# Kernel tuning notes

Hardware: AMD Instinct MI355X
Metric: run time of the kernel (lower is better)

The kernel has to match this reference:

```python
import jax, jax.numpy as jnp
import numpy as np
import math

GAMMA = 0.97      # discounting
LAM = 0.95        # gae lambda
EPSILON = 0.3     # ppo clip
EPS = 0.2         # gpo clip (eps)
ENT_COST = 0.01
RSCALE = 1.0
ALPHA = 1.0
NUM_STEPS = 1.0e6 # normalization step count buffer


def _mlp(x, Ws, bs):
    for i, (W, b) in enumerate(zip(Ws, bs)):
        x = x @ W.T + b
        if i < len(Ws) - 1:
            x = jax.nn.silu(x)
    return x


def _dist_create(logits):
    loc, s = jnp.split(logits, 2, axis=-1)
    return loc, jax.nn.softplus(s) + 0.001


def _log_det_jac(x):
    # tanh bijector log|det J| per element
    return 2.0 * (math.log(2.0) - x - jax.nn.softplus(-2.0 * x))


def _log_prob(loc, scale, dist):
    lu = -0.5 * jnp.square((dist - loc) / scale)
    ln = 0.5 * math.log(2.0 * math.pi) + jnp.log(scale)
    return (lu - ln - _log_det_jac(dist)).sum(-1)


def _entropy(loc, scale, noise):
    ln = 0.5 * math.log(2.0 * math.pi) + jnp.log(scale)
    ent = (0.5 + ln) * jnp.ones_like(loc)
    dist = loc + scale * noise  # reparameterized sample (torch.normal)
    return (ent + _log_det_jac(dist)).sum(-1)


def _kl(pl, ps, ql, qs):
    vr = jnp.square(ps / qs)
    t1 = jnp.square((pl - ql) / qs)
    return (0.5 * (vr + t1 - 1.0 - jnp.log(vr))).mean(-1)


def _normalize(obs, rm, rv):
    var = jnp.clip(rv / (NUM_STEPS + 1.0), 1e-6, 1e6)
    return jnp.clip((obs - rm) / jnp.sqrt(var), -5.0, 5.0)


def _gae(truncation, termination, reward, values, bootstrap_value):
    tm = 1.0 - truncation
    v1 = jnp.concatenate([values[1:], bootstrap_value[None]], 0)
    deltas = (reward + GAMMA * (1.0 - termination) * v1 - values) * tm

    def step(acc, xs):
        d, te, tmask = xs
        acc = d + GAMMA * (1.0 - te) * tmask * LAM * acc
        return acc, acc

    _, vmx = jax.lax.scan(step, jnp.zeros_like(bootstrap_value),
                          (deltas, termination, tm), reverse=True)
    vs = vmx + values
    vs1 = jnp.concatenate([vs[1:], bootstrap_value[None]], 0)
    adv = (reward + GAMMA * (1.0 - termination) * vs1 - values) * tm
    return vs, adv


def _loss(observation, pobservation, reward, done, truncation, logits, action,
          noise, pw0, pb0, pw1, pb1, pw2, pb2, vw0, vb0, vw1, vb1, vw2, vb2,
          running_mean, running_variance, kl_coef):
    sg = jax.lax.stop_gradient
    Pw, Pb = [pw0, pw1, pw2], [pb0, pb1, pb2]
    Vw, Vb = [vw0, vw1, vw2], [vb0, vb1, vb2]

    obs_n = _normalize(observation, running_mean, running_variance)
    pobs_n = _normalize(pobservation, running_mean, running_variance)

    guider_logits = _mlp(obs_n[:-1], Pw, Pb)
    learner_logits = _mlp(pobs_n[:-1], Pw, Pb)
    baseline = _mlp(obs_n, Vw, Vb).squeeze(-1)  # [T+1, B]
    bootstrap = baseline[-1]
    baseline = baseline[:-1]

    reward_s = reward * RSCALE
    termination = done * (1.0 - truncation)

    loc, scale = _dist_create(logits)
    b_lp = _log_prob(loc, scale, action)
    gl, gs = _dist_create(guider_logits)
    g_lp = _log_prob(gl, gs, action)
    ll, ls = _dist_create(learner_logits)
    l_lp = _log_prob(ll, ls, action)

    kl_learner = _kl(sg(gl), sg(gs), ll, ls).mean()
    kl_guider = _kl(gl, gs, sg(ll), sg(ls))
    # use_clip = True branch
    diff = g_lp - l_lp
    m = jnp.where(diff > math.log(1.0 + EPS), 1.0,
                  jnp.where(diff < math.log(1.0 - EPS), 1.0, 0.0))
    kl_guider = (kl_guider * m).mean()

    vs, adv = _gae(truncation, termination, reward_s, sg(baseline), sg(bootstrap))
    vs = sg(vs)
    adv = sg((adv - adv.mean()) / (jnp.std(adv, ddof=1) + 1e-5))

    rho = jnp.exp(g_lp - b_lp)
    rho_clip = jnp.exp(jnp.clip(g_lp - sg(l_lp), math.log(1.0 - EPS), math.log(1.0 + EPS))
                       + sg(l_lp) - b_lp)
    rho_clip = jnp.clip(rho_clip, 1.0 - EPSILON, 1.0 + EPSILON)
    guider_policy_loss = -jnp.mean(jnp.minimum(rho * adv, rho_clip * adv))

    rho2 = jnp.exp(jnp.minimum(l_lp - b_lp, 10.0))  # stable_exp
    rho2c = jnp.clip(rho2, 1.0 - EPSILON, 1.0 + EPSILON)
    learner_policy_loss = -jnp.mean(jnp.minimum(rho2 * adv, rho2c * adv))

    v_err = vs - baseline
    v_loss = jnp.mean(v_err * v_err) * 0.25

    entropy = jnp.mean(_entropy(loc, scale, noise))
    entropy_loss = -ENT_COST * entropy

    learner_loss = kl_learner + learner_policy_loss * ALPHA  # use_clip
    guider_loss = kl_guider + guider_policy_loss
    total = learner_loss + guider_loss + v_loss + entropy_loss
    return total, guider_loss, learner_loss, kl_learner


def setup_inputs() -> dict:
    key = jax.random.key(0)
    T, B, OBS, ACT, H = 1024, 256, 64, 8, 256
    ks = iter(jax.random.split(key, 32))

    def lin(fin, fout):
        W = jax.random.normal(next(ks), (fout, fin), jnp.float32) / np.float32(np.sqrt(fin))
        b = jnp.zeros((fout,), jnp.float32)
        return W, b

    pw0, pb0 = lin(OBS, H); pw1, pb1 = lin(H, H); pw2, pb2 = lin(H, 2 * ACT)
    vw0, vb0 = lin(OBS, H); vw1, vb1 = lin(H, H); vw2, vb2 = lin(H, 1)

    observation = jax.random.normal(next(ks), (T + 1, B, OBS), jnp.float32)
    pobservation = observation + 0.1 * jax.random.normal(next(ks), (T + 1, B, OBS), jnp.float32)
    reward = jax.random.normal(next(ks), (T, B), jnp.float32)
    done = (jax.random.uniform(next(ks), (T, B)) < 0.01).astype(jnp.float32)
    truncation = (jax.random.uniform(next(ks), (T, B)) < 0.005).astype(jnp.float32)
    logits = 0.5 * jax.random.normal(next(ks), (T, B, 2 * ACT), jnp.float32)
    action = jax.random.normal(next(ks), (T, B, ACT), jnp.float32)
    noise = jax.random.normal(next(ks), (T, B, ACT), jnp.float32)
    running_mean = jnp.zeros((OBS,), jnp.float32)
    running_variance = jnp.ones((OBS,), jnp.float32) * NUM_STEPS  # unit variance after /num_steps
    kl_coef = jnp.ones((1,), jnp.float32)

    return {"observation": observation, "pobservation": pobservation,
            "reward": reward, "done": done, "truncation": truncation,
            "logits": logits, "action": action, "noise": noise,
            "pw0": pw0, "pb0": pb0, "pw1": pw1, "pb1": pb1, "pw2": pw2, "pb2": pb2,
            "vw0": vw0, "vb0": vb0, "vw1": vw1, "vb1": vb1, "vw2": vw2, "vb2": vb2,
            "running_mean": running_mean, "running_variance": running_variance,
            "kl_coef": kl_coef}


def reference(observation, pobservation, reward, done, truncation, logits, action,
              noise, pw0, pb0, pw1, pb1, pw2, pb2, vw0, vb0, vw1, vb1, vw2, vb2,
              running_mean, running_variance, kl_coef):
    return _loss(observation, pobservation, reward, done, truncation, logits,
                 action, noise, pw0, pb0, pw1, pb1, pw2, pb2, vw0, vb0, vw1, vb1,
                 vw2, vb2, running_mean, running_variance, kl_coef)
```

## Files before the change

kernel.cpp:

```cpp
#include <hip/hip_runtime.h>
#include <math.h>

#define GAMMA_   0.97f
#define LAM_     0.95f
#define EPSILON_ 0.3f
#define HLOG2PI_ 0.91893853320467274f
#define LOG2C_   0.69314718055994531f
#define LOG1P2_  0.18232155679395463f
#define LOG0P8_  (-0.22314355131420976f)

typedef unsigned short u16;
typedef unsigned int   u32;
typedef _Float16 half8 __attribute__((ext_vector_type(8)));
typedef _Float16 half4 __attribute__((ext_vector_type(4)));
typedef __attribute__((ext_vector_type(4))) float floatx4;
typedef __attribute__((ext_vector_type(8))) float floatx8;

constexpr int  TT     = 1024;
constexpr long ROWS_P = (long)TT * 256;
constexpr long ROWS_V = (long)(TT + 1) * 256;

constexpr long FR_W0P_HI = 0;
constexpr long FR_W0P_LO = 16384;
constexpr long FR_W1P_HI = 32768;
constexpr long FR_W1P_LO = 98304;
constexpr long FR_W2P_HI = 163840;
constexpr long FR_W2P_LO = 167936;
constexpr long FR_W0V_HI = 172032;
constexpr long FR_W0V_LO = 188416;
constexpr long FR_W1V_HI = 204800;
constexpr long FR_W1V_LO = 270336;
constexpr long FR_W2V_HI = 335872;
constexpr long FR_W2V_LO = 339968;
constexpr long FR_TOTAL  = 344064;

constexpr long WS_ACC  = 0;
constexpr long WS_INV  = 32;
constexpr long WS_ADV  = 96;
constexpr long WS_BASE = WS_ADV + ROWS_P;
constexpr long WS_GA   = WS_BASE + ROWS_V;
constexpr long WS_GP   = WS_GA + 8192;
constexpr long WS_GS   = WS_GP + 8192;
constexpr long WS_BANK = WS_GS + 8192;


__device__ __forceinline__ float softplus_f(float x) {
  return (x > 20.f) ? x : log1pf(expf(x));
}
__device__ __forceinline__ float silu_f(float x) {
  return x * __builtin_amdgcn_rcpf(1.f + __expf(-x));
}
__device__ __forceinline__ float clamp30(float x) {
  return fminf(1e30f, fmaxf(-1e30f, x));
}

__global__ void prep_kernel(const float* __restrict__ rv,
                            float* __restrict__ inv_std,
                            float* __restrict__ accum,
                            float* __restrict__ accumB) {
  int t = threadIdx.x;
  if (t < 32) accum[t] = 0.f;
  for (int i = t; i < 1024; i += 256) accumB[i] = 0.f;
  if (t < 64) {
    float var = rv[t] / 1000001.0f;
    var = fminf(1e6f, fmaxf(1e-6f, var));
    inv_std[t] = 1.f / sqrtf(var);
  }
}

__global__ void convert_kernel(const float* __restrict__ pw0,
                               const float* __restrict__ pw1,
                               const float* __restrict__ pw2,
                               const float* __restrict__ vw0,
                               const float* __restrict__ vw1,
                               const float* __restrict__ vw2,
                               u16* __restrict__ frag) {
  int idx = blockIdx.x * 256 + threadIdx.x;
  const float* W; int kslog, K, nvalid; long hioff, looff; int e;
  if (idx < 16384)       { W = pw0; e = idx;          kslog = 1; K = 64;  nvalid = 256; hioff = FR_W0P_HI; looff = FR_W0P_LO; }
  else if (idx < 81920)  { W = pw1; e = idx - 16384;  kslog = 3; K = 256; nvalid = 256; hioff = FR_W1P_HI; looff = FR_W1P_LO; }
  else if (idx < 86016)  { W = pw2; e = idx - 81920;  kslog = 3; K = 256; nvalid = 16;  hioff = FR_W2P_HI; looff = FR_W2P_LO; }
  else if (idx < 102400) { W = vw0; e = idx - 86016;  kslog = 1; K = 64;  nvalid = 256; hioff = FR_W0V_HI; looff = FR_W0V_LO; }
  else if (idx < 167936) { W = vw1; e = idx - 102400; kslog = 3; K = 256; nvalid = 256; hioff = FR_W1V_HI; looff = FR_W1V_LO; }
  else                   { W = vw2; e = idx - 167936; kslog = 3; K = 256; nvalid = 1;   hioff = FR_W2V_HI; looff = FR_W2V_LO; }
  int j    = e & 7;
  int lane = (e >> 3) & 63;
  int ks   = (e >> 9) & ((1 << kslog) - 1);
  int nt   = e >> (9 + kslog);
  int n = nt * 16 + (lane & 15);
  int k = ks * 32 + ((lane >> 4) << 3) + j;
  float w = (n < nvalid) ? W[n * K + k] : 0.f;
  _Float16 hi = (_Float16)w;
  _Float16 lo = (_Float16)(w - (float)hi);
  frag[hioff + e] = *(u16*)&hi;
  frag[looff + e] = *(u16*)&lo;
}

constexpr int SX = 72;
constexpr int SH = 264;

__global__ __launch_bounds__(256, 5)
void policy_kernel(const float* __restrict__ obs,
                   const float* __restrict__ pobs,
                   const float* __restrict__ rm,
                   const float* __restrict__ inv_std,
                   const u16* __restrict__ frag,
                   const float* __restrict__ b0,
                   const float* __restrict__ b1,
                   const float* __restrict__ b2,
                   const float* __restrict__ logits,
                   const float* __restrict__ action,
                   const float* __restrict__ noise,
                   const float* __restrict__ adv,
                   const float* __restrict__ accum,
                   float* __restrict__ accumB) {
  __shared__ __align__(16) _Float16 H[32 * SH];
  __shared__ __align__(16) float OUT2[2 * 32 * 16];
  __shared__ float red[80];

  const int tid  = threadIdx.x;
  const long row0 = (long)blockIdx.x * 16;
  const int lane = tid & 63;
  const int wv   = tid >> 6;
  const int lm   = lane & 15;
  const int lq   = lane >> 4;

  _Float16* X = H;

  {
    int vr = tid >> 3;
    int f0 = (tid & 7) * 8;
    const float* src = (vr < 16) ? obs : pobs;
    floatx8 v  = *(const floatx8*)&src[(row0 + (vr & 15)) * 64 + f0];
    floatx8 m  = *(const floatx8*)&rm[f0];
    floatx8 is = *(const floatx8*)&inv_std[f0];
    half8 h;
    #pragma unroll
    for (int j = 0; j < 8; ++j)
      h[j] = (_Float16)fminf(5.f, fmaxf(-5.f, (v[j] - m[j]) * is[j]));
    *(half8*)&X[vr * SX + f0] = h;
  }

  const int  er   = (tid >> 3) & 15;
  const int  ed   = tid & 7;
  const long erow = row0 + er;
  float pf_a   = action[erow * 8 + ed];
  float pf_loc = logits[erow * 16 + ed];
  float pf_sr  = logits[erow * 16 + 8 + ed];
  float pf_nd  = noise[erow * 8 + ed];
  float pf_adv = adv[erow];
  float pf_s3  = accum[3];
  float pf_s4  = accum[4];

  floatx4 acc[2][4];
  #pragma unroll
  for (int nt = 0; nt < 4; ++nt) {
    floatx4 bz = *(const floatx4*)&b0[(wv * 4 + nt) * 16 + lq * 4];
    acc[0][nt] = bz; acc[1][nt] = bz;
  }
  __syncthreads();

  {
    const half8* B0h = (const half8*)(frag + FR_W0P_HI);
    const half8* B0l = (const half8*)(frag + FR_W0P_LO);
    #pragma unroll
    for (int ks = 0; ks < 2; ++ks) {
      half8 Bh[4], Bl[4];
      #pragma unroll
      for (int nt = 0; nt < 4; ++nt) {
        int ntg = wv * 4 + nt;
        Bh[nt] = B0h[(ntg * 2 + ks) * 64 + lane];
        Bl[nt] = B0l[(ntg * 2 + ks) * 64 + lane];
      }
      half8 A0 = *(const half8*)&X[lm * SX + ks * 32 + lq * 8];
      half8 A1 = *(const half8*)&X[(16 + lm) * SX + ks * 32 + lq * 8];
      __builtin_amdgcn_s_setprio(1);
      #pragma unroll
      for (int nt = 0; nt < 4; ++nt) {
        acc[0][nt] = __builtin_amdgcn_mfma_f32_16x16x32_f16(Bh[nt], A0, acc[0][nt], 0, 0, 0);
        acc[1][nt] = __builtin_amdgcn_mfma_f32_16x16x32_f16(Bh[nt], A1, acc[1][nt], 0, 0, 0);
      }
      #pragma unroll
      for (int nt = 0; nt < 4; ++nt) {
        acc[0][nt] = __builtin_amdgcn_mfma_f32_16x16x32_f16(Bl[nt], A0, acc[0][nt], 0, 0, 0);
        acc[1][nt] = __builtin_amdgcn_mfma_f32_16x16x32_f16(Bl[nt], A1, acc[1][nt], 0, 0, 0);
      }
      __builtin_amdgcn_s_setprio(0);
    }
  }
  __syncthreads();

  #pragma unroll
  for (int nt = 0; nt < 4; ++nt) {
    int colbase = (wv * 4 + nt) * 16 + lq * 4;
    #pragma unroll
    for (int mt = 0; mt < 2; ++mt) {
      int row = mt * 16 + lm;
      half4 h;
      #pragma unroll
      for (int reg = 0; reg < 4; ++reg)
        h[reg] = (_Float16)silu_f(acc[mt][nt][reg]);
      *(half4*)&H[row * SH + colbase] = h;
    }
  }
  __syncthreads();

  {
    const half8* B1h = (const half8*)(frag + FR_W1P_HI);
    const half8* B1l = (const half8*)(frag + FR_W1P_LO);
    #pragma unroll
    for (int nt = 0; nt < 4; ++nt) {
      floatx4 bz = *(const floatx4*)&b1[(wv * 4 + nt) * 16 + lq * 4];
      acc[0][nt] = bz; acc[1][nt] = bz;
    }
    #pragma unroll 1
    for (int ks = 0; ks < 8; ++ks) {
      half8 Bh[4], Bl[4];
      #pragma unroll
      for (int nt = 0; nt < 4; ++nt) {
        int ntg = wv * 4 + nt;
        Bh[nt] = B1h[(ntg * 8 + ks) * 64 + lane];
        Bl[nt] = B1l[(ntg * 8 + ks) * 64 + lane];
      }
      half8 A0 = *(const half8*)&H[lm * SH + ks * 32 + lq * 8];
      half8 A1 = *(const half8*)&H[(16 + lm) * SH + ks * 32 + lq * 8];
      __builtin_amdgcn_s_setprio(1);
      #pragma unroll
      for (int nt = 0; nt < 4; ++nt) {
        acc[0][nt] = __builtin_amdgcn_mfma_f32_16x16x32_f16(Bh[nt], A0, acc[0][nt], 0, 0, 0);
        acc[1][nt] = __builtin_amdgcn_mfma_f32_16x16x32_f16(Bh[nt], A1, acc[1][nt], 0, 0, 0);
      }
      #pragma unroll
      for (int nt = 0; nt < 4; ++nt) {
        acc[0][nt] = __builtin_amdgcn_mfma_f32_16x16x32_f16(Bl[nt], A0, acc[0][nt], 0, 0, 0);
        acc[1][nt] = __builtin_amdgcn_mfma_f32_16x16x32_f16(Bl[nt], A1, acc[1][nt], 0, 0, 0);
      }
      __builtin_amdgcn_s_setprio(0);
    }
  }
  __syncthreads();

  #pragma unroll
  for (int nt = 0; nt < 4; ++nt) {
    int colbase = (wv * 4 + nt) * 16 + lq * 4;
    #pragma unroll
    for (int mt = 0; mt < 2; ++mt) {
      int row = mt * 16 + lm;
      half4 h;
      #pragma unroll
      for (int reg = 0; reg < 4; ++reg)
        h[reg] = (_Float16)silu_f(acc[mt][nt][reg]);
      *(half4*)&H[row * SH + colbase] = h;
    }
  }
  __syncthreads();

  {
    const half8* B2h = (const half8*)(frag + FR_W2P_HI);
    const half8* B2l = (const half8*)(frag + FR_W2P_LO);
    const int m3 = wv & 1, kh = wv >> 1;
    floatx4 c3a, c3b = (floatx4){0.f, 0.f, 0.f, 0.f};
    c3a = (kh == 0) ? *(const floatx4*)&b2[lq * 4] : (floatx4){0.f, 0.f, 0.f, 0.f};
    __builtin_amdgcn_s_setprio(1);
    #pragma unroll
    for (int j = 0; j < 4; j += 2) {
      int ks = kh * 4 + j;
      half8 A0 = *(const half8*)&H[(m3 * 16 + lm) * SH + ks * 32 + lq * 8];
      half8 A1 = *(const half8*)&H[(m3 * 16 + lm) * SH + (ks + 1) * 32 + lq * 8];
      c3a = __builtin_amdgcn_mfma_f32_16x16x32_f16(B2h[ks * 64 + lane],       A0, c3a, 0, 0, 0);
      c3b = __builtin_amdgcn_mfma_f32_16x16x32_f16(B2h[(ks + 1) * 64 + lane], A1, c3b, 0, 0, 0);
      c3a = __builtin_amdgcn_mfma_f32_16x16x32_f16(B2l[ks * 64 + lane],       A0, c3a, 0, 0, 0);
      c3b = __builtin_amdgcn_mfma_f32_16x16x32_f16(B2l[(ks + 1) * 64 + lane], A1, c3b, 0, 0, 0);
    }
    __builtin_amdgcn_s_setprio(0);
    *(floatx4*)&OUT2[kh * 512 + (m3 * 16 + lm) * 16 + lq * 4] = c3a + c3b;
  }
  __syncthreads();

  if (tid < 128) {
    int r = tid >> 3;
    int d = tid & 7;

    float gl  = OUT2[r * 16 + d]            + OUT2[512 + r * 16 + d];
    float gsr = OUT2[r * 16 + 8 + d]        + OUT2[512 + r * 16 + 8 + d];
    float ll  = OUT2[(16 + r) * 16 + d]     + OUT2[512 + (16 + r) * 16 + d];
    float lsr = OUT2[(16 + r) * 16 + 8 + d] + OUT2[512 + (16 + r) * 16 + 8 + d];
    float a   = pf_a;
    float loc = pf_loc;
    float sr  = pf_sr;
    float nd  = pf_nd;

    float gs = softplus_f(gsr) + 1e-3f;
    float ls = softplus_f(lsr) + 1e-3f;
    float sc = softplus_f(sr) + 1e-3f;
    float ldj = 2.f * (LOG2C_ - a - softplus_f(-2.f * a));
    float lgs = logf(gs), lls = logf(ls), lsc = logf(sc);
    float zg = (a - gl) / gs;
    float zl = (a - ll) / ls;
    float z  = (a - loc) / sc;
    float glp = -0.5f * zg * zg - lgs - HLOG2PI_ - ldj;
    float llp = -0.5f * zl * zl - lls - HLOG2PI_ - ldj;
    float blp = -0.5f * z * z - lsc - HLOG2PI_ - ldj;
    float ratio = gs / ls;
    float vr = ratio * ratio;
    float t1 = (gl - ll) / ls; t1 *= t1;
    float kl = 0.5f * (vr + t1 - 1.f) - (lgs - lls);
    float dist = loc + sc * nd;
    float ent = 0.5f + HLOG2PI_ + lsc
              + 2.f * (LOG2C_ - dist - softplus_f(-2.f * dist));

    #pragma unroll
    for (int o = 4; o > 0; o >>= 1) {
      glp += __shfl_down(glp, o, 8);
      llp += __shfl_down(llp, o, 8);
      blp += __shfl_down(blp, o, 8);
      kl  += __shfl_down(kl, o, 8);
      ent += __shfl_down(ent, o, 8);
    }

    if (d == 0) {
      kl *= 0.125f;
      kl  = clamp30(kl);
      ent = clamp30(ent);

      float diff = glp - llp;
      float m = (diff > LOG1P2_ || diff < LOG0P8_) ? 1.f : 0.f;

      float N = (float)ROWS_P;
      float sum = pf_s3, sumsq = pf_s4;
      float mean = sum / N;
      float var  = fmaxf((sumsq - sum * sum / N) / (N - 1.f), 0.f);
      float inv  = 1.f / (sqrtf(var) + 1e-5f);
      float a_n  = (pf_adv - mean) * inv;

      float rho = expf(fminf(glp - blp, 80.f));
      float cl  = fminf(LOG1P2_, fmaxf(LOG0P8_, diff));
      float rc  = expf(fminf(cl + llp - blp, 80.f));
      rc = fminf(1.f + EPSILON_, fmaxf(1.f - EPSILON_, rc));
      float gp = clamp30(fminf(rho * a_n, rc * a_n));

      float rho2 = expf(fminf(llp - blp, 10.f));
      float r2c  = fminf(1.f + EPSILON_, fmaxf(1.f - EPSILON_, rho2));
      float lp = clamp30(fminf(rho2 * a_n, r2c * a_n));

      red[r]      = kl;
      red[16 + r] = kl * m;
      red[32 + r] = ent;
      red[48 + r] = gp;
      red[64 + r] = lp;
    }
  }
  __syncthreads();
  if (tid < 16) {
    float s0 = red[tid], s1 = red[16 + tid], s2 = red[32 + tid];
    float s3 = red[48 + tid], s4 = red[64 + tid];
    #pragma unroll
    for (int o = 8; o > 0; o >>= 1) {
      s0 += __shfl_down(s0, o, 16);
      s1 += __shfl_down(s1, o, 16);
      s2 += __shfl_down(s2, o, 16);
      s3 += __shfl_down(s3, o, 16);
      s4 += __shfl_down(s4, o, 16);
    }
    if (tid == 0) {
      float* bank = accumB + (blockIdx.x & 31) * 32;
      atomicAdd(&bank[0], s0);
      atomicAdd(&bank[1], s1);
      atomicAdd(&bank[2], s2);
      atomicAdd(&bank[6], s3);
      atomicAdd(&bank[7], s4);
    }
  }
}

__global__ __launch_bounds__(256, 5)
void value_kernel(const float* __restrict__ obs,
                  const float* __restrict__ rm,
                  const float* __restrict__ inv_std,
                  const u16* __restrict__ frag,
                  const float* __restrict__ b0,
                  const float* __restrict__ b1,
                  const float* __restrict__ b2,
                  float* __restrict__ baseline) {
  __shared__ __align__(16) _Float16 H[32 * SH];
  __shared__ float OUT2V[64];

  const int tid  = threadIdx.x;
  const long row0 = (long)blockIdx.x * 32;
  const int lane = tid & 63;
  const int wv   = tid >> 6;
  const int lm   = lane & 15;
  const int lq   = lane >> 4;

  _Float16* X = H;

  {
    int vr = tid >> 3;
    int f0 = (tid & 7) * 8;
    floatx8 v  = *(const floatx8*)&obs[(row0 + vr) * 64 + f0];
    floatx8 m  = *(const floatx8*)&rm[f0];
    floatx8 is = *(const floatx8*)&inv_std[f0];
    half8 h;
    #pragma unroll
    for (int j = 0; j < 8; ++j)
      h[j] = (_Float16)fminf(5.f, fmaxf(-5.f, (v[j] - m[j]) * is[j]));
    *(half8*)&X[vr * SX + f0] = h;
  }

  floatx4 acc[2][4];
  #pragma unroll
  for (int nt = 0; nt < 4; ++nt) {
    floatx4 bz = *(const floatx4*)&b0[(wv * 4 + nt) * 16 + lq * 4];
    acc[0][nt] = bz; acc[1][nt] = bz;
  }
  __syncthreads();

  {
    const half8* B0h = (const half8*)(frag + FR_W0V_HI);
    const half8* B0l = (const half8*)(frag + FR_W0V_LO);
    #pragma unroll
    for (int ks = 0; ks < 2; ++ks) {
      half8 Bh[4], Bl[4];
      #pragma unroll
      for (int nt = 0; nt < 4; ++nt) {
        int ntg = wv * 4 + nt;
        Bh[nt] = B0h[(ntg * 2 + ks) * 64 + lane];
        Bl[nt] = B0l[(ntg * 2 + ks) * 64 + lane];
      }
      half8 A0 = *(const half8*)&X[lm * SX + ks * 32 + lq * 8];
      half8 A1 = *(const half8*)&X[(16 + lm) * SX + ks * 32 + lq * 8];
      __builtin_amdgcn_s_setprio(1);
      #pragma unroll
      for (int nt = 0; nt < 4; ++nt) {
        acc[0][nt] = __builtin_amdgcn_mfma_f32_16x16x32_f16(Bh[nt], A0, acc[0][nt], 0, 0, 0);
        acc[1][nt] = __builtin_amdgcn_mfma_f32_16x16x32_f16(Bh[nt], A1, acc[1][nt], 0, 0, 0);
      }
      #pragma unroll
      for (int nt = 0; nt < 4; ++nt) {
        acc[0][nt] = __builtin_amdgcn_mfma_f32_16x16x32_f16(Bl[nt], A0, acc[0][nt], 0, 0, 0);
        acc[1][nt] = __builtin_amdgcn_mfma_f32_16x16x32_f16(Bl[nt], A1, acc[1][nt], 0, 0, 0);
      }
      __builtin_amdgcn_s_setprio(0);
    }
  }
  __syncthreads();

  #pragma unroll
  for (int nt = 0; nt < 4; ++nt) {
    int colbase = (wv * 4 + nt) * 16 + lq * 4;
    #pragma unroll
    for (int mt = 0; mt < 2; ++mt) {
      int row = mt * 16 + lm;
      half4 h;
      #pragma unroll
      for (int reg = 0; reg < 4; ++reg)
        h[reg] = (_Float16)silu_f(acc[mt][nt][reg]);
      *(half4*)&H[row * SH + colbase] = h;
    }
  }
  __syncthreads();

  {
    const half8* B1h = (const half8*)(frag + FR_W1V_HI);
    const half8* B1l = (const half8*)(frag + FR_W1V_LO);
    #pragma unroll
    for (int nt = 0; nt < 4; ++nt) {
      floatx4 bz = *(const floatx4*)&b1[(wv * 4 + nt) * 16 + lq * 4];
      acc[0][nt] = bz; acc[1][nt] = bz;
    }
    #pragma unroll 1
    for (int ks = 0; ks < 8; ++ks) {
      half8 Bh[4], Bl[4];
      #pragma unroll
      for (int nt = 0; nt < 4; ++nt) {
        int ntg = wv * 4 + nt;
        Bh[nt] = B1h[(ntg * 8 + ks) * 64 + lane];
        Bl[nt] = B1l[(ntg * 8 + ks) * 64 + lane];
      }
      half8 A0 = *(const half8*)&H[lm * SH + ks * 32 + lq * 8];
      half8 A1 = *(const half8*)&H[(16 + lm) * SH + ks * 32 + lq * 8];
      __builtin_amdgcn_s_setprio(1);
      #pragma unroll
      for (int nt = 0; nt < 4; ++nt) {
        acc[0][nt] = __builtin_amdgcn_mfma_f32_16x16x32_f16(Bh[nt], A0, acc[0][nt], 0, 0, 0);
        acc[1][nt] = __builtin_amdgcn_mfma_f32_16x16x32_f16(Bh[nt], A1, acc[1][nt], 0, 0, 0);
      }
      #pragma unroll
      for (int nt = 0; nt < 4; ++nt) {
        acc[0][nt] = __builtin_amdgcn_mfma_f32_16x16x32_f16(Bl[nt], A0, acc[0][nt], 0, 0, 0);
        acc[1][nt] = __builtin_amdgcn_mfma_f32_16x16x32_f16(Bl[nt], A1, acc[1][nt], 0, 0, 0);
      }
      __builtin_amdgcn_s_setprio(0);
    }
  }
  __syncthreads();

  #pragma unroll
  for (int nt = 0; nt < 4; ++nt) {
    int colbase = (wv * 4 + nt) * 16 + lq * 4;
    #pragma unroll
    for (int mt = 0; mt < 2; ++mt) {
      int row = mt * 16 + lm;
      half4 h;
      #pragma unroll
      for (int reg = 0; reg < 4; ++reg)
        h[reg] = (_Float16)silu_f(acc[mt][nt][reg]);
      *(half4*)&H[row * SH + colbase] = h;
    }
  }
  __syncthreads();

  {
    const half8* B2h = (const half8*)(frag + FR_W2V_HI);
    const half8* B2l = (const half8*)(frag + FR_W2V_LO);
    const int m3 = wv & 1, kh = wv >> 1;
    float bz = (kh == 0 && lq == 0) ? b2[0] : 0.f;
    floatx4 c3a = (floatx4){bz, 0.f, 0.f, 0.f};
    floatx4 c3b = (floatx4){0.f, 0.f, 0.f, 0.f};
    __builtin_amdgcn_s_setprio(1);
    #pragma unroll
    for (int j = 0; j < 4; j += 2) {
      int ks = kh * 4 + j;
      half8 A0 = *(const half8*)&H[(m3 * 16 + lm) * SH + ks * 32 + lq * 8];
      half8 A1 = *(const half8*)&H[(m3 * 16 + lm) * SH + (ks + 1) * 32 + lq * 8];
      c3a = __builtin_amdgcn_mfma_f32_16x16x32_f16(B2h[ks * 64 + lane],       A0, c3a, 0, 0, 0);
      c3b = __builtin_amdgcn_mfma_f32_16x16x32_f16(B2h[(ks + 1) * 64 + lane], A1, c3b, 0, 0, 0);
      c3a = __builtin_amdgcn_mfma_f32_16x16x32_f16(B2l[ks * 64 + lane],       A0, c3a, 0, 0, 0);
      c3b = __builtin_amdgcn_mfma_f32_16x16x32_f16(B2l[(ks + 1) * 64 + lane], A1, c3b, 0, 0, 0);
    }
    __builtin_amdgcn_s_setprio(0);
    if (lq == 0) OUT2V[kh * 32 + m3 * 16 + lm] = c3a[0] + c3b[0];
  }
  __syncthreads();

  if (tid < 32) baseline[row0 + tid] = OUT2V[tid] + OUT2V[32 + tid];
}

__global__ void gae_phase1(const float* __restrict__ reward,
                           const float* __restrict__ done,
                           const float* __restrict__ trunc,
                           const float* __restrict__ baseline,
                           float* __restrict__ A, float* __restrict__ P) {
  int s = blockIdx.x, b = threadIdx.x;
  float Aa = 0.f, Pp = 1.f;
  for (int t = (s + 1) * 32 - 1; t >= s * 32; --t) {
    int idx = t * 256 + b;
    float r = reward[idx], d = done[idx], tr = trunc[idx];
    float tm = 1.f - tr;
    float te = d * tm;
    float bl = baseline[idx], bl1 = baseline[idx + 256];
    float g1 = GAMMA_ * (1.f - te);
    float delta = (r + g1 * bl1 - bl) * tm;
    float c = g1 * tm * LAM_;
    Aa = delta + c * Aa;
    Pp = c * Pp;
  }
  A[s * 256 + b] = Aa;
  P[s * 256 + b] = Pp;
}

__global__ void gae_phase2(const float* __restrict__ A,
                           const float* __restrict__ P,
                           float* __restrict__ seedv) {
  int b = threadIdx.x;
  float acc = 0.f;
  for (int s = 31; s >= 0; --s) {
    seedv[s * 256 + b] = acc;
    acc = A[s * 256 + b] + P[s * 256 + b] * acc;
  }
}

__global__ void gae_phase3(const float* __restrict__ reward,
                           const float* __restrict__ done,
                           const float* __restrict__ trunc,
                           const float* __restrict__ baseline,
                           const float* __restrict__ seedv,
                           float* __restrict__ adv,
                           float* __restrict__ accum) {
  __shared__ float red[12];
  int s = blockIdx.x, b = threadIdx.x;
  float acc = seedv[s * 256 + b];
  int tend = (s + 1) * 32;
  float vnext = baseline[tend * 256 + b];
  float vs_next = acc + vnext;
  float sa = 0.f, sa2 = 0.f, sv2 = 0.f;
  for (int t = tend - 1; t >= s * 32; --t) {
    int idx = t * 256 + b;
    float r = reward[idx], d = done[idx], tr = trunc[idx];
    float tm = 1.f - tr;
    float te = d * tm;
    float bl = baseline[idx];
    float g1 = GAMMA_ * (1.f - te);
    float delta = (r + g1 * vnext - bl) * tm;
    acc = delta + g1 * tm * LAM_ * acc;
    float at = (r + g1 * vs_next - bl) * tm;
    at = fminf(1e15f, fmaxf(-1e15f, at));
    adv[idx] = at;
    sa += at; sa2 += at * at;
    sv2 += fminf(acc * acc, 1e30f);
    vs_next = acc + bl;
    vnext = bl;
  }
  float v0 = sa, v1 = sa2, v2 = sv2;
  #pragma unroll
  for (int o = 32; o > 0; o >>= 1) {
    v0 += __shfl_down(v0, o, 64);
    v1 += __shfl_down(v1, o, 64);
    v2 += __shfl_down(v2, o, 64);
  }
  int lane = threadIdx.x & 63, w = threadIdx.x >> 6;
  if (lane == 0) { red[w] = v0; red[4 + w] = v1; red[8 + w] = v2; }
  __syncthreads();
  if (threadIdx.x == 0) {
    float s0=0.f, s1=0.f, s2=0.f;
    for (int q = 0; q < 4; ++q) { s0 += red[q]; s1 += red[4+q]; s2 += red[8+q]; }
    atomicAdd(&accum[3], s0);
    atomicAdd(&accum[4], s1);
    atomicAdd(&accum[5], s2);
  }
}

__global__ void finalize_kernel(const float* __restrict__ accum,
                                const float* __restrict__ accumB,
                                float* __restrict__ out) {
  int t = threadIdx.x;
  float s0 = 0.f, s1 = 0.f, s2 = 0.f, s6 = 0.f, s7 = 0.f;
  if (t < 32) {
    const float* bank = accumB + t * 32;
    s0 = bank[0]; s1 = bank[1]; s2 = bank[2]; s6 = bank[6]; s7 = bank[7];
  }
  #pragma unroll
  for (int o = 16; o > 0; o >>= 1) {
    s0 += __shfl_down(s0, o, 64);
    s1 += __shfl_down(s1, o, 64);
    s2 += __shfl_down(s2, o, 64);
    s6 += __shfl_down(s6, o, 64);
    s7 += __shfl_down(s7, o, 64);
  }
  if (t == 0) {
    float N = (float)ROWS_P;
    float kl_learner = s0 / N;
    float kl_guider  = s1 / N;
    float entropy    = s2 / N;
    float v_loss     = 0.25f * accum[5] / N;
    float gp_loss    = -s6 / N;
    float lp_loss    = -s7 / N;
    float learner_loss = kl_learner + lp_loss;
    float guider_loss  = kl_guider + gp_loss;
    float total = learner_loss + guider_loss + v_loss - 0.01f * entropy;
    out[0] = total;
    out[1] = guider_loss;
    out[2] = learner_loss;
    out[3] = kl_learner;
  }
}

extern "C" void kernel_launch(void* const* d_in, const int* in_sizes, int n_in,
                              void* d_out, int out_size, void* d_ws, size_t ws_size,
                              hipStream_t stream) {
  (void)in_sizes; (void)n_in; (void)out_size; (void)ws_size;
  const float* obs    = (const float*)d_in[0];
  const float* pobs   = (const float*)d_in[1];
  const float* reward = (const float*)d_in[2];
  const float* done   = (const float*)d_in[3];
  const float* trunc  = (const float*)d_in[4];
  const float* logits = (const float*)d_in[5];
  const float* action = (const float*)d_in[6];
  const float* noise  = (const float*)d_in[7];
  const float* pw0 = (const float*)d_in[8];
  const float* pb0 = (const float*)d_in[9];
  const float* pw1 = (const float*)d_in[10];
  const float* pb1 = (const float*)d_in[11];
  const float* pw2 = (const float*)d_in[12];
  const float* pb2 = (const float*)d_in[13];
  const float* vw0 = (const float*)d_in[14];
  const float* vb0 = (const float*)d_in[15];
  const float* vw1 = (const float*)d_in[16];
  const float* vb1 = (const float*)d_in[17];
  const float* vw2 = (const float*)d_in[18];
  const float* vb2 = (const float*)d_in[19];
  const float* rm  = (const float*)d_in[20];
  const float* rv  = (const float*)d_in[21];

  u16*   frag  = (u16*)d_ws;
  float* fbase = (float*)d_ws + FR_TOTAL / 2;
  float* accum   = fbase + WS_ACC;
  float* inv_std = fbase + WS_INV;
  float* adv     = fbase + WS_ADV;
  float* base    = fbase + WS_BASE;
  float* gA      = fbase + WS_GA;
  float* gP      = fbase + WS_GP;
  float* gS      = fbase + WS_GS;
  float* accumB  = fbase + WS_BANK;
  float* out = (float*)d_out;

  prep_kernel<<<1, 256, 0, stream>>>(rv, inv_std, accum, accumB);
  convert_kernel<<<672, 256, 0, stream>>>(pw0, pw1, pw2, vw0, vw1, vw2, frag);

  value_kernel<<<(int)(ROWS_V / 32), 256, 0, stream>>>(
      obs, rm, inv_std, frag, vb0, vb1, vb2, base);

  gae_phase1<<<32, 256, 0, stream>>>(reward, done, trunc, base, gA, gP);
  gae_phase2<<<1, 256, 0, stream>>>(gA, gP, gS);
  gae_phase3<<<32, 256, 0, stream>>>(reward, done, trunc, base, gS, adv, accum);

  policy_kernel<<<(int)(ROWS_P / 16), 256, 0, stream>>>(
      obs, pobs, rm, inv_std, frag, pb0, pb1, pb2,
      logits, action, noise, adv, accum, accumB);

  finalize_kernel<<<1, 64, 0, stream>>>(accum, accumB, out);
}
```

Measured before the change: 583.9 us.

## Double rows per block and use 8 waves with 4x2 MFMA tiles

Both the policy and value MLP kernels now run 512 threads per block and process twice as many rows per block (64 stacked rows instead of 32). Each wave computes 4 row tiles by 2 column tiles instead of 2 by 4, so every fetched weight fragment is reused across more rows and total global weight traffic per row is halved. The cost is larger shared memory per block, more accumulator registers per wave, a reworked reduction over 32 rows, and fewer blocks in the grid.

```diff
diff --git a/kernel.cpp b/kernel.cpp
--- a/kernel.cpp
+++ b/kernel.cpp
@@ -99,7 +99,7 @@
 constexpr int SX = 72;
 constexpr int SH = 264;
 
-__global__ __launch_bounds__(256, 5)
+__global__ __launch_bounds__(512, 6)
 void policy_kernel(const float* __restrict__ obs,
                    const float* __restrict__ pobs,
                    const float* __restrict__ rm,
@@ -114,12 +114,12 @@
                    const float* __restrict__ adv,
                    const float* __restrict__ accum,
                    float* __restrict__ accumB) {
-  __shared__ __align__(16) _Float16 H[32 * SH];
-  __shared__ __align__(16) float OUT2[2 * 32 * 16];
-  __shared__ float red[80];
+  __shared__ __align__(16) _Float16 H[64 * SH];
+  __shared__ __align__(16) float OUT2[2 * 64 * 16];
+  __shared__ float red[160];
 
   const int tid  = threadIdx.x;
-  const long row0 = (long)blockIdx.x * 16;
+  const long row0 = (long)blockIdx.x * 32;
   const int lane = tid & 63;
   const int wv   = tid >> 6;
   const int lm   = lane & 15;
@@ -130,8 +130,8 @@
   {
     int vr = tid >> 3;
     int f0 = (tid & 7) * 8;
-    const float* src = (vr < 16) ? obs : pobs;
-    floatx8 v  = *(const floatx8*)&src[(row0 + (vr & 15)) * 64 + f0];
+    const float* src = (vr < 32) ? obs : pobs;
+    floatx8 v  = *(const floatx8*)&src[(row0 + (vr & 31)) * 64 + f0];
     floatx8 m  = *(const floatx8*)&rm[f0];
     floatx8 is = *(const floatx8*)&inv_std[f0];
     half8 h;
@@ -141,22 +141,26 @@
     *(half8*)&X[vr * SX + f0] = h;
   }
 
-  const int  er   = (tid >> 3) & 15;
-  const int  ed   = tid & 7;
-  const long erow = row0 + er;
-  float pf_a   = action[erow * 8 + ed];
-  float pf_loc = logits[erow * 16 + ed];
-  float pf_sr  = logits[erow * 16 + 8 + ed];
-  float pf_nd  = noise[erow * 8 + ed];
-  float pf_adv = adv[erow];
-  float pf_s3  = accum[3];
-  float pf_s4  = accum[4];
-
-  floatx4 acc[2][4];
+  float pf_a = 0.f, pf_loc = 0.f, pf_sr = 0.f, pf_nd = 0.f, pf_adv = 0.f;
+  if (tid < 256) {
+    const int  er   = tid >> 3;
+    const int  ed   = tid & 7;
+    const long erow = row0 + er;
+    pf_a   = action[erow * 8 + ed];
+    pf_loc = logits[erow * 16 + ed];
+    pf_sr  = logits[erow * 16 + 8 + ed];
+    pf_nd  = noise[erow * 8 + ed];
+    pf_adv = adv[erow];
+  }
+  float pf_s3 = accum[3];
+  float pf_s4 = accum[4];
+
+  floatx4 acc[4][2];
   #pragma unroll
-  for (int nt = 0; nt < 4; ++nt) {
-    floatx4 bz = *(const floatx4*)&b0[(wv * 4 + nt) * 16 + lq * 4];
-    acc[0][nt] = bz; acc[1][nt] = bz;
+  for (int nt = 0; nt < 2; ++nt) {
+    floatx4 bz = *(const floatx4*)&b0[(wv * 2 + nt) * 16 + lq * 4];
+    #pragma unroll
+    for (int mt = 0; mt < 4; ++mt) acc[mt][nt] = bz;
   }
   __syncthreads();
 
@@ -165,36 +169,38 @@
     const half8* B0l = (const half8*)(frag + FR_W0P_LO);
     #pragma unroll
     for (int ks = 0; ks < 2; ++ks) {
-      half8 Bh[4], Bl[4];
-      #pragma unroll
-      for (int nt = 0; nt < 4; ++nt) {
-        int ntg = wv * 4 + nt;
+      half8 Bh[2], Bl[2];
+      #pragma unroll
+      for (int nt = 0; nt < 2; ++nt) {
+        int ntg = wv * 2 + nt;
         Bh[nt] = B0h[(ntg * 2 + ks) * 64 + lane];
         Bl[nt] = B0l[(ntg * 2 + ks) * 64 + lane];
       }
-      half8 A0 = *(const half8*)&X[lm * SX + ks * 32 + lq * 8];
-      half8 A1 = *(const half8*)&X[(16 + lm) * SX + ks * 32 + lq * 8];
+      half8 A[4];
+      #pragma unroll
+      for (int mt = 0; mt < 4; ++mt)
+        A[mt] = *(const half8*)&X[(mt * 16 + lm) * SX + ks * 32 + lq * 8];
       __builtin_amdgcn_s_setprio(1);
       #pragma unroll
-      for (int nt = 0; nt < 4; ++nt) {
-        acc[0][nt] = __builtin_amdgcn_mfma_f32_16x16x32_f16(Bh[nt], A0, acc[0][nt], 0, 0, 0);
-        acc[1][nt] = __builtin_amdgcn_mfma_f32_16x16x32_f16(Bh[nt], A1, acc[1][nt], 0, 0, 0);
-      }
-      #pragma unroll
-      for (int nt = 0; nt < 4; ++nt) {
-        acc[0][nt] = __builtin_amdgcn_mfma_f32_16x16x32_f16(Bl[nt], A0, acc[0][nt], 0, 0, 0);
-        acc[1][nt] = __builtin_amdgcn_mfma_f32_16x16x32_f16(Bl[nt], A1, acc[1][nt], 0, 0, 0);
-      }
+      for (int mt = 0; mt < 4; ++mt)
+        #pragma unroll
+        for (int nt = 0; nt < 2; ++nt)
+          acc[mt][nt] = __builtin_amdgcn_mfma_f32_16x16x32_f16(Bh[nt], A[mt], acc[mt][nt], 0, 0, 0);
+      #pragma unroll
+      for (int mt = 0; mt < 4; ++mt)
+        #pragma unroll
+        for (int nt = 0; nt < 2; ++nt)
+          acc[mt][nt] = __builtin_amdgcn_mfma_f32_16x16x32_f16(Bl[nt], A[mt], acc[mt][nt], 0, 0, 0);
       __builtin_amdgcn_s_setprio(0);
     }
   }
   __syncthreads();
 
   #pragma unroll
-  for (int nt = 0; nt < 4; ++nt) {
-    int colbase = (wv * 4 + nt) * 16 + lq * 4;
-    #pragma unroll
-    for (int mt = 0; mt < 2; ++mt) {
+  for (int nt = 0; nt < 2; ++nt) {
+    int colbase = (wv * 2 + nt) * 16 + lq * 4;
+    #pragma unroll
+    for (int mt = 0; mt < 4; ++mt) {
       int row = mt * 16 + lm;
       half4 h;
       #pragma unroll
@@ -209,42 +215,45 @@
     const half8* B1h = (const half8*)(frag + FR_W1P_HI);
     const half8* B1l = (const half8*)(frag + FR_W1P_LO);
     #pragma unroll
-    for (int nt = 0; nt < 4; ++nt) {
-      floatx4 bz = *(const floatx4*)&b1[(wv * 4 + nt) * 16 + lq * 4];
-      acc[0][nt] = bz; acc[1][nt] = bz;
+    for (int nt = 0; nt < 2; ++nt) {
+      floatx4 bz = *(const floatx4*)&b1[(wv * 2 + nt) * 16 + lq * 4];
+      #pragma unroll
+      for (int mt = 0; mt < 4; ++mt) acc[mt][nt] = bz;
     }
     #pragma unroll 1
     for (int ks = 0; ks < 8; ++ks) {
-      half8 Bh[4], Bl[4];
-      #pragma unroll
-      for (int nt = 0; nt < 4; ++nt) {
-        int ntg = wv * 4 + nt;
+      half8 Bh[2], Bl[2];
+      #pragma unroll
+      for (int nt = 0; nt < 2; ++nt) {
+        int ntg = wv * 2 + nt;
         Bh[nt] = B1h[(ntg * 8 + ks) * 64 + lane];
         Bl[nt] = B1l[(ntg * 8 + ks) * 64 + lane];
       }
-      half8 A0 = *(const half8*)&H[lm * SH + ks * 32 + lq * 8];
-      half8 A1 = *(const half8*)&H[(16 + lm) * SH + ks * 32 + lq * 8];
+      half8 A[4];
+      #pragma unroll
+      for (int mt = 0; mt < 4; ++mt)
+        A[mt] = *(const half8*)&H[(mt * 16 + lm) * SH + ks * 32 + lq * 8];
       __builtin_amdgcn_s_setprio(1);
       #pragma unroll
-      for (int nt = 0; nt < 4; ++nt) {
-        acc[0][nt] = __builtin_amdgcn_mfma_f32_16x16x32_f16(Bh[nt], A0, acc[0][nt], 0, 0, 0);
-        acc[1][nt] = __builtin_amdgcn_mfma_f32_16x16x32_f16(Bh[nt], A1, acc[1][nt], 0, 0, 0);
-      }
-      #pragma unroll
-      for (int nt = 0; nt < 4; ++nt) {
-        acc[0][nt] = __builtin_amdgcn_mfma_f32_16x16x32_f16(Bl[nt], A0, acc[0][nt], 0, 0, 0);
-        acc[1][nt] = __builtin_amdgcn_mfma_f32_16x16x32_f16(Bl[nt], A1, acc[1][nt], 0, 0, 0);
-      }
+      for (int mt = 0; mt < 4; ++mt)
+        #pragma unroll
+        for (int nt = 0; nt < 2; ++nt)
+          acc[mt][nt] = __builtin_amdgcn_mfma_f32_16x16x32_f16(Bh[nt], A[mt], acc[mt][nt], 0, 0, 0);
+      #pragma unroll
+      for (int mt = 0; mt < 4; ++mt)
+        #pragma unroll
+        for (int nt = 0; nt < 2; ++nt)
+          acc[mt][nt] = __builtin_amdgcn_mfma_f32_16x16x32_f16(Bl[nt], A[mt], acc[mt][nt], 0, 0, 0);
       __builtin_amdgcn_s_setprio(0);
     }
   }
   __syncthreads();
 
   #pragma unroll
-  for (int nt = 0; nt < 4; ++nt) {
-    int colbase = (wv * 4 + nt) * 16 + lq * 4;
-    #pragma unroll
-    for (int mt = 0; mt < 2; ++mt) {
+  for (int nt = 0; nt < 2; ++nt) {
+    int colbase = (wv * 2 + nt) * 16 + lq * 4;
+    #pragma unroll
+    for (int mt = 0; mt < 4; ++mt) {
       int row = mt * 16 + lm;
       half4 h;
       #pragma unroll
@@ -258,7 +267,7 @@
   {
     const half8* B2h = (const half8*)(frag + FR_W2P_HI);
     const half8* B2l = (const half8*)(frag + FR_W2P_LO);
-    const int m3 = wv & 1, kh = wv >> 1;
+    const int m3 = wv & 3, kh = wv >> 2;
     floatx4 c3a, c3b = (floatx4){0.f, 0.f, 0.f, 0.f};
     c3a = (kh == 0) ? *(const floatx4*)&b2[lq * 4] : (floatx4){0.f, 0.f, 0.f, 0.f};
     __builtin_amdgcn_s_setprio(1);
@@ -273,18 +282,18 @@
       c3b = __builtin_amdgcn_mfma_f32_16x16x32_f16(B2l[(ks + 1) * 64 + lane], A1, c3b, 0, 0, 0);
     }
     __builtin_amdgcn_s_setprio(0);
-    *(floatx4*)&OUT2[kh * 512 + (m3 * 16 + lm) * 16 + lq * 4] = c3a + c3b;
-  }
-  __syncthreads();
-
-  if (tid < 128) {
+    *(floatx4*)&OUT2[kh * 1024 + (m3 * 16 + lm) * 16 + lq * 4] = c3a + c3b;
+  }
+  __syncthreads();
+
+  if (tid < 256) {
     int r = tid >> 3;
     int d = tid & 7;
 
-    float gl  = OUT2[r * 16 + d]            + OUT2[512 + r * 16 + d];
-    float gsr = OUT2[r * 16 + 8 + d]        + OUT2[512 + r * 16 + 8 + d];
-    float ll  = OUT2[(16 + r) * 16 + d]     + OUT2[512 + (16 + r) * 16 + d];
-    float lsr = OUT2[(16 + r) * 16 + 8 + d] + OUT2[512 + (16 + r) * 16 + 8 + d];
+    float gl  = OUT2[r * 16 + d]            + OUT2[1024 + r * 16 + d];
+    float gsr = OUT2[r * 16 + 8 + d]        + OUT2[1024 + r * 16 + 8 + d];
+    float ll  = OUT2[(32 + r) * 16 + d]     + OUT2[1024 + (32 + r) * 16 + d];
+    float lsr = OUT2[(32 + r) * 16 + 8 + d] + OUT2[1024 + (32 + r) * 16 + 8 + d];
     float a   = pf_a;
     float loc = pf_loc;
     float sr  = pf_sr;
@@ -343,24 +352,24 @@
       float r2c  = fminf(1.f + EPSILON_, fmaxf(1.f - EPSILON_, rho2));
       float lp = clamp30(fminf(rho2 * a_n, r2c * a_n));
 
-      red[r]      = kl;
-      red[16 + r] = kl * m;
-      red[32 + r] = ent;
-      red[48 + r] = gp;
-      red[64 + r] = lp;
-    }
-  }
-  __syncthreads();
-  if (tid < 16) {
-    float s0 = red[tid], s1 = red[16 + tid], s2 = red[32 + tid];
-    float s3 = red[48 + tid], s4 = red[64 + tid];
-    #pragma unroll
-    for (int o = 8; o > 0; o >>= 1) {
-      s0 += __shfl_down(s0, o, 16);
-      s1 += __shfl_down(s1, o, 16);
-      s2 += __shfl_down(s2, o, 16);
-      s3 += __shfl_down(s3, o, 16);
-      s4 += __shfl_down(s4, o, 16);
+      red[r]       = kl;
+      red[32 + r]  = kl * m;
+      red[64 + r]  = ent;
+      red[96 + r]  = gp;
+      red[128 + r] = lp;
+    }
+  }
+  __syncthreads();
+  if (tid < 32) {
+    float s0 = red[tid], s1 = red[32 + tid], s2 = red[64 + tid];
+    float s3 = red[96 + tid], s4 = red[128 + tid];
+    #pragma unroll
+    for (int o = 16; o > 0; o >>= 1) {
+      s0 += __shfl_down(s0, o, 32);
+      s1 += __shfl_down(s1, o, 32);
+      s2 += __shfl_down(s2, o, 32);
+      s3 += __shfl_down(s3, o, 32);
+      s4 += __shfl_down(s4, o, 32);
     }
     if (tid == 0) {
       float* bank = accumB + (blockIdx.x & 31) * 32;
@@ -373,7 +382,7 @@
   }
 }
 
-__global__ __launch_bounds__(256, 5)
+__global__ __launch_bounds__(512, 6)
 void value_kernel(const float* __restrict__ obs,
                   const float* __restrict__ rm,
                   const float* __restrict__ inv_std,
@@ -382,11 +391,11 @@
                   const float* __restrict__ b1,
                   const float* __restrict__ b2,
                   float* __restrict__ baseline) {
-  __shared__ __align__(16) _Float16 H[32 * SH];
-  __shared__ float OUT2V[64];
+  __shared__ __align__(16) _Float16 H[64 * SH];
+  __shared__ float OUT2V[128];
 
   const int tid  = threadIdx.x;
-  const long row0 = (long)blockIdx.x * 32;
+  const long row0 = (long)blockIdx.x * 64;
   const int lane = tid & 63;
   const int wv   = tid >> 6;
   const int lm   = lane & 15;
@@ -407,11 +416,12 @@
     *(half8*)&X[vr * SX + f0] = h;
   }
 
-  floatx4 acc[2][4];
+  floatx4 acc[4][2];
   #pragma unroll
-  for (int nt = 0; nt < 4; ++nt) {
-    floatx4 bz = *(const floatx4*)&b0[(wv * 4 + nt) * 16 + lq * 4];
-    acc[0][nt] = bz; acc[1][nt] = bz;
+  for (int nt = 0; nt < 2; ++nt) {
+    floatx4 bz = *(const floatx4*)&b0[(wv * 2 + nt) * 16 + lq * 4];
+    #pragma unroll
+    for (int mt = 0; mt < 4; ++mt) acc[mt][nt] = bz;
   }
   __syncthreads();
 
@@ -420,36 +430,38 @@
     const half8* B0l = (const half8*)(frag + FR_W0V_LO);
     #pragma unroll
     for (int ks = 0; ks < 2; ++ks) {
-      half8 Bh[4], Bl[4];
-      #pragma unroll
-      for (int nt = 0; nt < 4; ++nt) {
-        int ntg = wv * 4 + nt;
+      half8 Bh[2], Bl[2];
+      #pragma unroll
+      for (int nt = 0; nt < 2; ++nt) {
+        int ntg = wv * 2 + nt;
         Bh[nt] = B0h[(ntg * 2 + ks) * 64 + lane];
         Bl[nt] = B0l[(ntg * 2 + ks) * 64 + lane];
       }
-      half8 A0 = *(const half8*)&X[lm * SX + ks * 32 + lq * 8];
-      half8 A1 = *(const half8*)&X[(16 + lm) * SX + ks * 32 + lq * 8];
+      half8 A[4];
+      #pragma unroll
+      for (int mt = 0; mt < 4; ++mt)
+        A[mt] = *(const half8*)&X[(mt * 16 + lm) * SX + ks * 32 + lq * 8];
       __builtin_amdgcn_s_setprio(1);
       #pragma unroll
-      for (int nt = 0; nt < 4; ++nt) {
-        acc[0][nt] = __builtin_amdgcn_mfma_f32_16x16x32_f16(Bh[nt], A0, acc[0][nt], 0, 0, 0);
-        acc[1][nt] = __builtin_amdgcn_mfma_f32_16x16x32_f16(Bh[nt], A1, acc[1][nt], 0, 0, 0);
-      }
-      #pragma unroll
-      for (int nt = 0; nt < 4; ++nt) {
-        acc[0][nt] = __builtin_amdgcn_mfma_f32_16x16x32_f16(Bl[nt], A0, acc[0][nt], 0, 0, 0);
-        acc[1][nt] = __builtin_amdgcn_mfma_f32_16x16x32_f16(Bl[nt], A1, acc[1][nt], 0, 0, 0);
-      }
+      for (int mt = 0; mt < 4; ++mt)
+        #pragma unroll
+        for (int nt = 0; nt < 2; ++nt)
+          acc[mt][nt] = __builtin_amdgcn_mfma_f32_16x16x32_f16(Bh[nt], A[mt], acc[mt][nt], 0, 0, 0);
+      #pragma unroll
+      for (int mt = 0; mt < 4; ++mt)
+        #pragma unroll
+        for (int nt = 0; nt < 2; ++nt)
+          acc[mt][nt] = __builtin_amdgcn_mfma_f32_16x16x32_f16(Bl[nt], A[mt], acc[mt][nt], 0, 0, 0);
       __builtin_amdgcn_s_setprio(0);
     }
   }
   __syncthreads();
 
   #pragma unroll
-  for (int nt = 0; nt < 4; ++nt) {
-    int colbase = (wv * 4 + nt) * 16 + lq * 4;
-    #pragma unroll
-    for (int mt = 0; mt < 2; ++mt) {
+  for (int nt = 0; nt < 2; ++nt) {
+    int colbase = (wv * 2 + nt) * 16 + lq * 4;
+    #pragma unroll
+    for (int mt = 0; mt < 4; ++mt) {
       int row = mt * 16 + lm;
       half4 h;
       #pragma unroll
@@ -464,42 +476,45 @@
     const half8* B1h = (const half8*)(frag + FR_W1V_HI);
     const half8* B1l = (const half8*)(frag + FR_W1V_LO);
     #pragma unroll
-    for (int nt = 0; nt < 4; ++nt) {
-      floatx4 bz = *(const floatx4*)&b1[(wv * 4 + nt) * 16 + lq * 4];
-      acc[0][nt] = bz; acc[1][nt] = bz;
+    for (int nt = 0; nt < 2; ++nt) {
+      floatx4 bz = *(const floatx4*)&b1[(wv * 2 + nt) * 16 + lq * 4];
+      #pragma unroll
+      for (int mt = 0; mt < 4; ++mt) acc[mt][nt] = bz;
     }
     #pragma unroll 1
     for (int ks = 0; ks < 8; ++ks) {
-      half8 Bh[4], Bl[4];
-      #pragma unroll
-      for (int nt = 0; nt < 4; ++nt) {
-        int ntg = wv * 4 + nt;
+      half8 Bh[2], Bl[2];
+      #pragma unroll
+      for (int nt = 0; nt < 2; ++nt) {
+        int ntg = wv * 2 + nt;
         Bh[nt] = B1h[(ntg * 8 + ks) * 64 + lane];
         Bl[nt] = B1l[(ntg * 8 + ks) * 64 + lane];
       }
-      half8 A0 = *(const half8*)&H[lm * SH + ks * 32 + lq * 8];
-      half8 A1 = *(const half8*)&H[(16 + lm) * SH + ks * 32 + lq * 8];
+      half8 A[4];
+      #pragma unroll
+      for (int mt = 0; mt < 4; ++mt)
+        A[mt] = *(const half8*)&H[(mt * 16 + lm) * SH + ks * 32 + lq * 8];
       __builtin_amdgcn_s_setprio(1);
       #pragma unroll
-      for (int nt = 0; nt < 4; ++nt) {
-        acc[0][nt] = __builtin_amdgcn_mfma_f32_16x16x32_f16(Bh[nt], A0, acc[0][nt], 0, 0, 0);
-        acc[1][nt] = __builtin_amdgcn_mfma_f32_16x16x32_f16(Bh[nt], A1, acc[1][nt], 0, 0, 0);
-      }
-      #pragma unroll
-      for (int nt = 0; nt < 4; ++nt) {
-        acc[0][nt] = __builtin_amdgcn_mfma_f32_16x16x32_f16(Bl[nt], A0, acc[0][nt], 0, 0, 0);
-        acc[1][nt] = __builtin_amdgcn_mfma_f32_16x16x32_f16(Bl[nt], A1, acc[1][nt], 0, 0, 0);
-      }
+      for (int mt = 0; mt < 4; ++mt)
+        #pragma unroll
+        for (int nt = 0; nt < 2; ++nt)
+          acc[mt][nt] = __builtin_amdgcn_mfma_f32_16x16x32_f16(Bh[nt], A[mt], acc[mt][nt], 0, 0, 0);
+      #pragma unroll
+      for (int mt = 0; mt < 4; ++mt)
+        #pragma unroll
+        for (int nt = 0; nt < 2; ++nt)
+          acc[mt][nt] = __builtin_amdgcn_mfma_f32_16x16x32_f16(Bl[nt], A[mt], acc[mt][nt], 0, 0, 0);
       __builtin_amdgcn_s_setprio(0);
     }
   }
   __syncthreads();
 
   #pragma unroll
-  for (int nt = 0; nt < 4; ++nt) {
-    int colbase = (wv * 4 + nt) * 16 + lq * 4;
-    #pragma unroll
-    for (int mt = 0; mt < 2; ++mt) {
+  for (int nt = 0; nt < 2; ++nt) {
+    int colbase = (wv * 2 + nt) * 16 + lq * 4;
+    #pragma unroll
+    for (int mt = 0; mt < 4; ++mt) {
       int row = mt * 16 + lm;
       half4 h;
       #pragma unroll
@@ -513,7 +528,7 @@
   {
     const half8* B2h = (const half8*)(frag + FR_W2V_HI);
     const half8* B2l = (const half8*)(frag + FR_W2V_LO);
-    const int m3 = wv & 1, kh = wv >> 1;
+    const int m3 = wv & 3, kh = wv >> 2;
     float bz = (kh == 0 && lq == 0) ? b2[0] : 0.f;
     floatx4 c3a = (floatx4){bz, 0.f, 0.f, 0.f};
     floatx4 c3b = (floatx4){0.f, 0.f, 0.f, 0.f};
@@ -529,11 +544,11 @@
       c3b = __builtin_amdgcn_mfma_f32_16x16x32_f16(B2l[(ks + 1) * 64 + lane], A1, c3b, 0, 0, 0);
     }
     __builtin_amdgcn_s_setprio(0);
-    if (lq == 0) OUT2V[kh * 32 + m3 * 16 + lm] = c3a[0] + c3b[0];
-  }
-  __syncthreads();
-
-  if (tid < 32) baseline[row0 + tid] = OUT2V[tid] + OUT2V[32 + tid];
+    if (lq == 0) OUT2V[kh * 64 + m3 * 16 + lm] = c3a[0] + c3b[0];
+  }
+  __syncthreads();
+
+  if (tid < 64) baseline[row0 + tid] = OUT2V[tid] + OUT2V[64 + tid];
 }
 
 __global__ void gae_phase1(const float* __restrict__ reward,
@@ -697,14 +712,14 @@
   prep_kernel<<<1, 256, 0, stream>>>(rv, inv_std, accum, accumB);
   convert_kernel<<<672, 256, 0, stream>>>(pw0, pw1, pw2, vw0, vw1, vw2, frag);
 
-  value_kernel<<<(int)(ROWS_V / 32), 256, 0, stream>>>(
+  value_kernel<<<(int)(ROWS_V / 64), 512, 0, stream>>>(
       obs, rm, inv_std, frag, vb0, vb1, vb2, base);
 
   gae_phase1<<<32, 256, 0, stream>>>(reward, done, trunc, base, gA, gP);
   gae_phase2<<<1, 256, 0, stream>>>(gA, gP, gS);
   gae_phase3<<<32, 256, 0, stream>>>(reward, done, trunc, base, gS, adv, accum);
 
-  policy_kernel<<<(int)(ROWS_P / 16), 256, 0, stream>>>(
+  policy_kernel<<<(int)(ROWS_P / 32), 512, 0, stream>>>(
       obs, pobs, rm, inv_std, frag, pb0, pb1, pb2,
       logits, action, noise, adv, accum, accumB);
 
```

Result: faster. 563.7 us (-3.5%).
